# Kernel tuning notes

Measured on AMD Instinct MI355X. Metric: run time of the kernel, lower is better.

The kernel has to match this reference:

```python
import jax, jax.numpy as jnp
import numpy as np

B, S, D, H, L, DFF, LAT, V, N = 256, 64, 512, 8, 6, 2048, 256, 16, 64


def _pe(s, d):
    pos = np.arange(s)[:, None].astype(np.float32)
    div = np.exp(np.arange(0, d, 2).astype(np.float32) * (-np.log(10000.0) / d))
    pe = np.zeros((s, d), np.float32)
    pe[:, 0::2] = np.sin(pos * div)
    pe[:, 1::2] = np.cos(pos * div)
    return jnp.asarray(pe)


def setup_inputs() -> dict:
    key = jax.random.key(0)
    ks = iter(jax.random.split(key, 64))
    def nrm(shape, scale):
        return jax.random.normal(next(ks), shape, jnp.float32) * scale
    d = {}
    d['latent'] = nrm((B, LAT), 1.0)
    ct = jax.random.randint(next(ks), (B, S), 0, V).astype(jnp.float32)
    na = jax.random.randint(next(ks), (B, S), 0, N).astype(jnp.float32)
    nb = jax.random.randint(next(ks), (B, S), 0, N).astype(jnp.float32)
    val = jax.random.normal(next(ks), (B, S), jnp.float32)
    d['teacher_seq'] = jnp.stack([ct, na, nb, val], -1)
    for g in ('gumbel_a', 'gumbel_b'):
        u = jax.random.uniform(next(ks), (B, S, N), jnp.float32, 1e-6, 1.0 - 1e-6)
        d[g] = -jnp.log(-jnp.log(u))
    dq = D // 4
    d['type_emb'] = nrm((V, dq), 0.02)
    d['node_a_emb'] = nrm((N, dq), 0.02)
    d['node_b_emb'] = nrm((N, dq), 0.02)
    d['value_w'] = nrm((dq, 1), 1.0); d['value_b'] = jnp.zeros((dq,))
    d['proj_w'] = nrm((D, D), D ** -0.5); d['proj_b'] = jnp.zeros((D,))
    d['latent_w'] = nrm((D, LAT), LAT ** -0.5); d['latent_b'] = jnp.zeros((D,))
    d['sa_in_w'] = nrm((L, 3 * D, D), D ** -0.5); d['sa_in_b'] = jnp.zeros((L, 3 * D))
    d['sa_out_w'] = nrm((L, D, D), D ** -0.5); d['sa_out_b'] = jnp.zeros((L, D))
    d['ca_q_w'] = nrm((L, D, D), D ** -0.5); d['ca_q_b'] = jnp.zeros((L, D))
    d['ca_kv_w'] = nrm((L, 2 * D, D), D ** -0.5); d['ca_kv_b'] = jnp.zeros((L, 2 * D))
    d['ca_out_w'] = nrm((L, D, D), D ** -0.5); d['ca_out_b'] = jnp.zeros((L, D))
    d['ff1_w'] = nrm((L, DFF, D), D ** -0.5); d['ff1_b'] = jnp.zeros((L, DFF))
    d['ff2_w'] = nrm((L, D, DFF), DFF ** -0.5); d['ff2_b'] = jnp.zeros((L, D))
    for nm in ('ln1', 'ln2', 'ln3'):
        d[nm + '_g'] = jnp.ones((L, D)); d[nm + '_b'] = jnp.zeros((L, D))
    d['type_w'] = nrm((V, D), D ** -0.5); d['type_b'] = jnp.zeros((V,))
    d['na_w'] = nrm((N, D), D ** -0.5); d['na_b'] = jnp.zeros((N,))
    d['val_w'] = nrm((1, D), D ** -0.5); d['val_b'] = jnp.zeros((1,))
    d['nb_w'] = nrm((N, D + N), (D + N) ** -0.5); d['nb_b'] = jnp.zeros((N,))
    return d


def _ln(x, g, b, eps=1e-5):
    m = x.mean(-1, keepdims=True)
    v = jnp.mean((x - m) ** 2, -1, keepdims=True)
    return (x - m) / jnp.sqrt(v + eps) * g + b


def _attn(xq, xkv, wq, bq, wk, bk, wv, bv, wo, bo, mask):
    b, sq, dm = xq.shape
    hd = dm // H
    q = (xq @ wq.T + bq).reshape(b, sq, H, hd)
    k = (xkv @ wk.T + bk).reshape(b, -1, H, hd)
    v = (xkv @ wv.T + bv).reshape(b, -1, H, hd)
    s = jnp.einsum('bqhd,bkhd->bhqk', q, k) / np.sqrt(hd).astype(np.float32)
    if mask is not None:
        s = s + mask
    a = jax.nn.softmax(s, -1)
    o = jnp.einsum('bhqk,bkhd->bqhd', a, v).reshape(b, sq, dm)
    return o @ wo.T + bo


def _forward(latent, teacher_seq, gumbel_a, gumbel_b, type_emb, node_a_emb, node_b_emb,
             value_w, value_b, proj_w, proj_b, latent_w, latent_b,
             sa_in_w, sa_in_b, sa_out_w, sa_out_b,
             ca_q_w, ca_q_b, ca_kv_w, ca_kv_b, ca_out_w, ca_out_b,
             ff1_w, ff1_b, ff2_w, ff2_b,
             ln1_g, ln1_b, ln2_g, ln2_b, ln3_g, ln3_b,
             type_w, type_b, na_w, na_b, val_w, val_b, nb_w, nb_b):
    s = teacher_seq.shape[1]
    memory = (latent @ latent_w.T + latent_b)[:, None, :]  # [B,1,D]
    ct = jnp.clip(teacher_seq[..., 0].astype(jnp.int32), 0, V - 1)
    na = jnp.clip(teacher_seq[..., 1].astype(jnp.int32), 0, N - 1)
    nb = jnp.clip(teacher_seq[..., 2].astype(jnp.int32), 0, N - 1)
    emb = jnp.concatenate([type_emb[ct], node_a_emb[na], node_b_emb[nb],
                           teacher_seq[..., 3:4] @ value_w.T + value_b], -1)
    x = emb @ proj_w.T + proj_b + _pe(s, D)
    mask = jnp.where(jnp.triu(jnp.ones((s, s), bool), 1), -jnp.inf, 0.0)
    for l in range(L):
        wq, wk, wv = jnp.split(sa_in_w[l], 3, 0)
        bq, bk, bv = jnp.split(sa_in_b[l], 3, 0)
        x = _ln(x + _attn(x, x, wq, bq, wk, bk, wv, bv, sa_out_w[l], sa_out_b[l], mask), ln1_g[l], ln1_b[l])
        wkc, wvc = jnp.split(ca_kv_w[l], 2, 0)
        bkc, bvc = jnp.split(ca_kv_b[l], 2, 0)
        x = _ln(x + _attn(x, memory, ca_q_w[l], ca_q_b[l], wkc, bkc, wvc, bvc, ca_out_w[l], ca_out_b[l], None), ln2_g[l], ln2_b[l])
        ff = jax.nn.relu(x @ ff1_w[l].T + ff1_b[l]) @ ff2_w[l].T + ff2_b[l]
        x = _ln(x + ff, ln3_g[l], ln3_b[l])
    type_logits = x @ type_w.T + type_b
    node_a_logits = x @ na_w.T + na_b
    values = x @ val_w.T + val_b
    # gumbel_softmax(logits, tau).argmax == argmax(logits + gumbel) (tau > 0)
    node_a_sample = jnp.argmax(node_a_logits + gumbel_a, -1)
    oh = jax.nn.one_hot(node_a_sample, N, dtype=x.dtype)
    node_b_logits = jnp.concatenate([x, oh], -1) @ nb_w.T + nb_b
    masked = jnp.where(oh > 0, -jnp.inf, node_b_logits)  # node_b != node_a constraint
    node_b_sample = jnp.argmax(masked + gumbel_b, -1)
    sequence = jnp.stack([jnp.argmax(type_logits, -1).astype(x.dtype),
                          node_a_sample.astype(x.dtype),
                          node_b_sample.astype(x.dtype),
                          values[..., 0]], -1)
    return type_logits, node_a_logits, node_b_logits, values, sequence


def reference(latent, teacher_seq, gumbel_a, gumbel_b, type_emb, node_a_emb, node_b_emb,
              value_w, value_b, proj_w, proj_b, latent_w, latent_b,
              sa_in_w, sa_in_b, sa_out_w, sa_out_b,
              ca_q_w, ca_q_b, ca_kv_w, ca_kv_b, ca_out_w, ca_out_b,
              ff1_w, ff1_b, ff2_w, ff2_b,
              ln1_g, ln1_b, ln2_g, ln2_b, ln3_g, ln3_b,
              type_w, type_b, na_w, na_b, val_w, val_b, nb_w, nb_b):
    return _forward(latent, teacher_seq, gumbel_a, gumbel_b, type_emb, node_a_emb, node_b_emb,
                    value_w, value_b, proj_w, proj_b, latent_w, latent_b,
                    sa_in_w, sa_in_b, sa_out_w, sa_out_b,
                    ca_q_w, ca_q_b, ca_kv_w, ca_kv_b, ca_out_w, ca_out_b,
                    ff1_w, ff1_b, ff2_w, ff2_b,
                    ln1_g, ln1_b, ln2_g, ln2_b, ln3_g, ln3_b,
                    type_w, type_b, na_w, na_b, val_w, val_b, nb_w, nb_b)
```

## Files before the change

kernel.cpp:

```cpp
#include <hip/hip_runtime.h>
#include <math.h>

#define BB    256
#define SS    64
#define DD    512
#define HH    8
#define LL    6
#define DFFc  2048
#define LATc  256
#define VVc   16
#define NNODE 64
#define TOK   (BB*SS)

typedef __attribute__((ext_vector_type(8))) _Float16 h8v;
typedef __attribute__((ext_vector_type(4))) float f4v;
typedef __attribute__((ext_vector_type(8))) unsigned short u16x8;

__device__ __forceinline__ float pe_val(int s, int c){
  const float kc = -9.2103403719761836f / 512.0f;
  float div = expf((float)(c & ~1) * kc);
  float arg = (float)s * div;
  return (c & 1) ? cosf(arg) : sinf(arg);
}

__device__ __forceinline__ unsigned short hbits(_Float16 h){
  union { _Float16 h; unsigned short u; } x; x.h = h; return x.u;
}
__device__ __forceinline__ void split4h(float4 v, ushort4& h0, ushort4& h1){
  _Float16 a0 = (_Float16)v.x; float r0 = v.x - (float)a0; h0.x = hbits(a0); h1.x = hbits((_Float16)r0);
  _Float16 a1 = (_Float16)v.y; float r1 = v.y - (float)a1; h0.y = hbits(a1); h1.y = hbits((_Float16)r1);
  _Float16 a2 = (_Float16)v.z; float r2 = v.z - (float)a2; h0.z = hbits(a2); h1.z = hbits((_Float16)r2);
  _Float16 a3 = (_Float16)v.w; float r3 = v.w - (float)a3; h0.w = hbits(a3); h1.w = hbits((_Float16)r3);
}
__device__ __forceinline__ u16x8 pack8(ushort4 a, ushort4 b){
  u16x8 r;
  r[0]=a.x; r[1]=a.y; r[2]=a.z; r[3]=a.w;
  r[4]=b.x; r[5]=b.y; r[6]=b.z; r[7]=b.w;
  return r;
}

__global__ __launch_bounds__(128) void emb_kernel(
    const float* __restrict__ ts, const float* __restrict__ te,
    const float* __restrict__ nae, const float* __restrict__ nbe,
    const float* __restrict__ vw, const float* __restrict__ vb,
    float* __restrict__ emb)
{
  const int tok = blockIdx.x;
  const int d   = threadIdx.x;
  float c0  = ts[(size_t)tok*4 + 0];
  float c1  = ts[(size_t)tok*4 + 1];
  float c2  = ts[(size_t)tok*4 + 2];
  float val = ts[(size_t)tok*4 + 3];
  int ct = min(max((int)c0, 0), VVc - 1);
  int na = min(max((int)c1, 0), NNODE - 1);
  int nb = min(max((int)c2, 0), NNODE - 1);
  float* er = emb + (size_t)tok * DD;
  er[d]       = te [ct*128 + d];
  er[128 + d] = nae[na*128 + d];
  er[256 + d] = nbe[nb*128 + d];
  er[384 + d] = val * vw[d] + vb[d];
}

template<int RELU, int ADDPE>
__global__ __launch_bounds__(256) void gemm_mfma(
    const float* __restrict__ A, const float* __restrict__ W,
    const float* __restrict__ bias, float* __restrict__ Cc,
    int M, int N, int K)
{
  __shared__ __attribute__((aligned(16))) unsigned short Ab[2][128][32];
  __shared__ __attribute__((aligned(16))) unsigned short Bb[2][128][32];
  const int n0 = blockIdx.x * 128;
  const int m0 = blockIdx.y * 128;
  const int t  = threadIdx.x;
  const int lane = t & 63;
  const int wave = t >> 6;
  const int wr = (wave >> 1) * 64;
  const int wc = (wave & 1) * 64;
  const int quad = lane >> 4;
  const int lc   = lane & 15;

  const int srow = t >> 1;
  const int skh  = (t & 1) * 16;

  const int ssw = ((srow ^ (srow >> 2)) & 3);
  const int p0  = (((t & 1) * 2) ^ ssw) * 8;
  const int p1  = ((((t & 1) * 2) ^ ssw) ^ 1) * 8;
  const int fo  = ((quad ^ ((lc ^ (lc >> 2)) & 3))) * 8;

  const float* ap = A + (size_t)(m0 + srow) * K + skh;
  const float* wp = W + (size_t)(n0 + srow) * K + skh;

  f4v acc[4][4];
  #pragma unroll
  for (int i = 0; i < 4; ++i)
    #pragma unroll
    for (int j = 0; j < 4; ++j) acc[i][j] = (f4v){0.f, 0.f, 0.f, 0.f};

  float4 va[4], vb[4];
  #pragma unroll
  for (int q = 0; q < 4; ++q) {
    va[q] = *(const float4*)(ap + q*4);
    vb[q] = *(const float4*)(wp + q*4);
  }

  for (int k0 = 0; k0 < K; k0 += 32) {
    __syncthreads();
    {
      ushort4 h0[4], h1[4];
      #pragma unroll
      for (int q = 0; q < 4; ++q) split4h(va[q], h0[q], h1[q]);
      *(u16x8*)&Ab[0][srow][p0] = pack8(h0[0], h0[1]);
      *(u16x8*)&Ab[0][srow][p1] = pack8(h0[2], h0[3]);
      *(u16x8*)&Ab[1][srow][p0] = pack8(h1[0], h1[1]);
      *(u16x8*)&Ab[1][srow][p1] = pack8(h1[2], h1[3]);
      #pragma unroll
      for (int q = 0; q < 4; ++q) split4h(vb[q], h0[q], h1[q]);
      *(u16x8*)&Bb[0][srow][p0] = pack8(h0[0], h0[1]);
      *(u16x8*)&Bb[0][srow][p1] = pack8(h0[2], h0[3]);
      *(u16x8*)&Bb[1][srow][p0] = pack8(h1[0], h1[1]);
      *(u16x8*)&Bb[1][srow][p1] = pack8(h1[2], h1[3]);
    }
    __syncthreads();
    if (k0 + 32 < K) {
      #pragma unroll
      for (int q = 0; q < 4; ++q) {
        va[q] = *(const float4*)(ap + k0 + 32 + q*4);
        vb[q] = *(const float4*)(wp + k0 + 32 + q*4);
      }
    }
    h8v af[2][4];
    #pragma unroll
    for (int mt = 0; mt < 4; ++mt)
      #pragma unroll
      for (int s = 0; s < 2; ++s)
        af[s][mt] = *(const h8v*)&Ab[s][wr + mt*16 + lc][fo];
    #pragma unroll
    for (int nt = 0; nt < 4; ++nt) {
      h8v b0 = *(const h8v*)&Bb[0][wc + nt*16 + lc][fo];
      h8v b1 = *(const h8v*)&Bb[1][wc + nt*16 + lc][fo];
      #pragma unroll
      for (int mt = 0; mt < 4; ++mt) {
        f4v c = acc[mt][nt];
        c = __builtin_amdgcn_mfma_f32_16x16x32_f16(af[1][mt], b1, c, 0, 0, 0);
        c = __builtin_amdgcn_mfma_f32_16x16x32_f16(af[1][mt], b0, c, 0, 0, 0);
        c = __builtin_amdgcn_mfma_f32_16x16x32_f16(af[0][mt], b1, c, 0, 0, 0);
        c = __builtin_amdgcn_mfma_f32_16x16x32_f16(af[0][mt], b0, c, 0, 0, 0);
        acc[mt][nt] = c;
      }
    }
  }
  #pragma unroll
  for (int mt = 0; mt < 4; ++mt)
    #pragma unroll
    for (int nt = 0; nt < 4; ++nt) {
      int col = n0 + wc + nt*16 + lc;
      float bvv = bias ? bias[col] : 0.f;
      #pragma unroll
      for (int r = 0; r < 4; ++r) {
        int row = m0 + wr + mt*16 + quad*4 + r;
        float v = acc[mt][nt][r] + bvv;
        if (RELU)  v = fmaxf(v, 0.f);
        if (ADDPE) v += pe_val(row & (SS - 1), col);
        Cc[(size_t)row * N + col] = v;
      }
    }
}

template<int RELU, int ADDPE>
__global__ __launch_bounds__(256) void gemm_mfma64(
    const float* __restrict__ A, const float* __restrict__ W,
    const float* __restrict__ bias, float* __restrict__ Cc,
    int M, int N, int K)
{
  __shared__ __attribute__((aligned(16))) unsigned short Ab[2][64][32];
  __shared__ __attribute__((aligned(16))) unsigned short Bb[2][128][32];
  const int n0 = blockIdx.x * 128;
  const int m0 = blockIdx.y * 64;
  const int t  = threadIdx.x;
  const int lane = t & 63;
  const int wave = t >> 6;
  const int wr = (wave >> 1) * 32;
  const int wc = (wave & 1) * 64;
  const int quad = lane >> 4;
  const int lc   = lane & 15;

  const int srow = t >> 1;
  const int skh  = (t & 1) * 16;
  const int ssw  = ((srow ^ (srow >> 2)) & 3);
  const int p0   = (((t & 1) * 2) ^ ssw) * 8;
  const int p1   = ((((t & 1) * 2) ^ ssw) ^ 1) * 8;
  const int arow = t >> 2;
  const int aq   = t & 3;
  const int pA   = (aq ^ ((arow ^ (arow >> 2)) & 3)) * 8;
  const int fo   = ((quad ^ ((lc ^ (lc >> 2)) & 3))) * 8;

  const float* ap = A + (size_t)(m0 + arow) * K + aq*8;
  const float* wp = W + (size_t)(n0 + srow) * K + skh;

  f4v acc[2][4];
  #pragma unroll
  for (int i = 0; i < 2; ++i)
    #pragma unroll
    for (int j = 0; j < 4; ++j) acc[i][j] = (f4v){0.f, 0.f, 0.f, 0.f};

  float4 va[2], vb[4];
  va[0] = *(const float4*)(ap);
  va[1] = *(const float4*)(ap + 4);
  #pragma unroll
  for (int q = 0; q < 4; ++q) vb[q] = *(const float4*)(wp + q*4);

  for (int k0 = 0; k0 < K; k0 += 32) {
    __syncthreads();
    {
      ushort4 h0[4], h1[4];
      split4h(va[0], h0[0], h1[0]);
      split4h(va[1], h0[1], h1[1]);
      *(u16x8*)&Ab[0][arow][pA] = pack8(h0[0], h0[1]);
      *(u16x8*)&Ab[1][arow][pA] = pack8(h1[0], h1[1]);
      #pragma unroll
      for (int q = 0; q < 4; ++q) split4h(vb[q], h0[q], h1[q]);
      *(u16x8*)&Bb[0][srow][p0] = pack8(h0[0], h0[1]);
      *(u16x8*)&Bb[0][srow][p1] = pack8(h0[2], h0[3]);
      *(u16x8*)&Bb[1][srow][p0] = pack8(h1[0], h1[1]);
      *(u16x8*)&Bb[1][srow][p1] = pack8(h1[2], h1[3]);
    }
    __syncthreads();
    if (k0 + 32 < K) {
      va[0] = *(const float4*)(ap + k0 + 32);
      va[1] = *(const float4*)(ap + k0 + 36);
      #pragma unroll
      for (int q = 0; q < 4; ++q) vb[q] = *(const float4*)(wp + k0 + 32 + q*4);
    }
    h8v af[2][2];
    #pragma unroll
    for (int mt = 0; mt < 2; ++mt)
      #pragma unroll
      for (int s = 0; s < 2; ++s)
        af[s][mt] = *(const h8v*)&Ab[s][wr + mt*16 + lc][fo];
    #pragma unroll
    for (int nt = 0; nt < 4; ++nt) {
      h8v b0 = *(const h8v*)&Bb[0][wc + nt*16 + lc][fo];
      h8v b1 = *(const h8v*)&Bb[1][wc + nt*16 + lc][fo];
      #pragma unroll
      for (int mt = 0; mt < 2; ++mt) {
        f4v c = acc[mt][nt];
        c = __builtin_amdgcn_mfma_f32_16x16x32_f16(af[1][mt], b1, c, 0, 0, 0);
        c = __builtin_amdgcn_mfma_f32_16x16x32_f16(af[1][mt], b0, c, 0, 0, 0);
        c = __builtin_amdgcn_mfma_f32_16x16x32_f16(af[0][mt], b1, c, 0, 0, 0);
        c = __builtin_amdgcn_mfma_f32_16x16x32_f16(af[0][mt], b0, c, 0, 0, 0);
        acc[mt][nt] = c;
      }
    }
  }
  #pragma unroll
  for (int mt = 0; mt < 2; ++mt)
    #pragma unroll
    for (int nt = 0; nt < 4; ++nt) {
      int col = n0 + wc + nt*16 + lc;
      float bvv = bias ? bias[col] : 0.f;
      #pragma unroll
      for (int r = 0; r < 4; ++r) {
        int row = m0 + wr + mt*16 + quad*4 + r;
        float v = acc[mt][nt][r] + bvv;
        if (RELU)  v = fmaxf(v, 0.f);
        if (ADDPE) v += pe_val(row & (SS - 1), col);
        Cc[(size_t)row * N + col] = v;
      }
    }
}

__global__ __launch_bounds__(256) void gemm64(
    const float* __restrict__ A, const float* __restrict__ W,
    const float* __restrict__ bias, float* __restrict__ Cc,
    int M, int N, int K)
{
  __shared__ float As[16][64];
  __shared__ float Bs[16][64];
  const int n0 = blockIdx.x * 64;
  const int m0 = blockIdx.y * 64;
  const int t  = threadIdx.x;
  const int tx = t & 15;
  const int ty = t >> 4;
  const int sr = t >> 2;
  const int sk = (t & 3) * 4;

  const float* ap = A + (size_t)(m0 + sr) * K + sk;
  const float* wp = W + (size_t)(n0 + sr) * K + sk;

  float acc[4][4];
  #pragma unroll
  for (int i = 0; i < 4; ++i)
    #pragma unroll
    for (int j = 0; j < 4; ++j) acc[i][j] = 0.f;

  float4 a = *(const float4*)ap;
  float4 b = *(const float4*)wp;
  for (int k0 = 0; k0 < K; k0 += 16) {
    __syncthreads();
    As[sk+0][sr]=a.x; As[sk+1][sr]=a.y; As[sk+2][sr]=a.z; As[sk+3][sr]=a.w;
    Bs[sk+0][sr]=b.x; Bs[sk+1][sr]=b.y; Bs[sk+2][sr]=b.z; Bs[sk+3][sr]=b.w;
    __syncthreads();
    if (k0 + 16 < K) {
      a = *(const float4*)(ap + k0 + 16);
      b = *(const float4*)(wp + k0 + 16);
    }
    #pragma unroll
    for (int kk = 0; kk < 16; ++kk) {
      float4 x = *(const float4*)&As[kk][ty*4];
      float4 y = *(const float4*)&Bs[kk][tx*4];
      float xv[4] = {x.x,x.y,x.z,x.w};
      float yv[4] = {y.x,y.y,y.z,y.w};
      #pragma unroll
      for (int i = 0; i < 4; ++i)
        #pragma unroll
        for (int j = 0; j < 4; ++j)
          acc[i][j] += xv[i] * yv[j];
    }
  }
  #pragma unroll
  for (int i = 0; i < 4; ++i) {
    int r = m0 + ty*4 + i;
    float* cp = Cc + (size_t)r * N + n0 + tx*4;
    float4 o;
    o.x = acc[i][0] + (bias ? bias[n0+tx*4+0] : 0.f);
    o.y = acc[i][1] + (bias ? bias[n0+tx*4+1] : 0.f);
    o.z = acc[i][2] + (bias ? bias[n0+tx*4+2] : 0.f);
    o.w = acc[i][3] + (bias ? bias[n0+tx*4+3] : 0.f);
    *(float4*)cp = o;
  }
}

__global__ __launch_bounds__(64) void attn_kernel(
    const float* __restrict__ qkv, float* __restrict__ out)
{
  const int b = blockIdx.x >> 3;
  const int h = blockIdx.x & 7;
  const int lane = threadIdx.x;
  __shared__ float4 ks[64][16];
  __shared__ float4 vs[64][16];
  const float* base = qkv + (size_t)(b*SS + lane) * (3*DD);
  #pragma unroll
  for (int dd = 0; dd < 16; ++dd) {
    ks[lane][dd] = *(const float4*)(base + DD     + h*64 + dd*4);
    vs[lane][dd] = *(const float4*)(base + 2*DD   + h*64 + dd*4);
  }
  float4 q4[16];
  #pragma unroll
  for (int dd = 0; dd < 16; ++dd) q4[dd] = *(const float4*)(base + h*64 + dd*4);
  __syncthreads();

  float s[64];
  float m = -1e30f;
  #pragma unroll
  for (int tk = 0; tk < 64; ++tk) {
    float acc = 0.f;
    #pragma unroll
    for (int dd = 0; dd < 16; ++dd) {
      float4 kv = ks[tk][dd];
      acc += q4[dd].x*kv.x + q4[dd].y*kv.y + q4[dd].z*kv.z + q4[dd].w*kv.w;
    }
    acc *= 0.125f;
    s[tk] = acc;
    if (tk <= lane && acc > m) m = acc;
  }
  float4 o4[16];
  #pragma unroll
  for (int dd = 0; dd < 16; ++dd) { o4[dd].x = 0.f; o4[dd].y = 0.f; o4[dd].z = 0.f; o4[dd].w = 0.f; }
  float l = 0.f;
  #pragma unroll
  for (int tk = 0; tk < 64; ++tk) {
    float w = (tk <= lane) ? expf(s[tk] - m) : 0.f;
    l += w;
    #pragma unroll
    for (int dd = 0; dd < 16; ++dd) {
      float4 vv = vs[tk][dd];
      o4[dd].x += w*vv.x; o4[dd].y += w*vv.y; o4[dd].z += w*vv.z; o4[dd].w += w*vv.w;
    }
  }
  float inv = 1.f / l;
  float* op = out + (size_t)(b*SS + lane) * DD + h*64;
  #pragma unroll
  for (int dd = 0; dd < 16; ++dd) {
    float4 vv; vv.x = o4[dd].x*inv; vv.y = o4[dd].y*inv; vv.z = o4[dd].z*inv; vv.w = o4[dd].w*inv;
    *(float4*)(op + dd*4) = vv;
  }
}

__global__ __launch_bounds__(256) void ln_kernel(
    float* __restrict__ x, const float* __restrict__ y,
    const float* __restrict__ g, const float* __restrict__ b, int ybcast)
{
  const int tok  = blockIdx.x * 4 + (threadIdx.x >> 6);
  const int lane = threadIdx.x & 63;
  float* xr = x + (size_t)tok * DD;
  const float* yr = y + (size_t)(ybcast ? (tok >> 6) : tok) * DD;
  const int c0 = lane * 8;
  float4 v0 = *(const float4*)(xr + c0);
  float4 v1 = *(const float4*)(xr + c0 + 4);
  float4 y0 = *(const float4*)(yr + c0);
  float4 y1 = *(const float4*)(yr + c0 + 4);
  float v[8] = {v0.x+y0.x, v0.y+y0.y, v0.z+y0.z, v0.w+y0.w,
                v1.x+y1.x, v1.y+y1.y, v1.z+y1.z, v1.w+y1.w};
  float sum = 0.f;
  #pragma unroll
  for (int i = 0; i < 8; ++i) sum += v[i];
  #pragma unroll
  for (int off = 32; off; off >>= 1) sum += __shfl_xor(sum, off);
  float mean = sum * (1.f / 512.f);
  float ss = 0.f;
  #pragma unroll
  for (int i = 0; i < 8; ++i) { float d = v[i] - mean; ss += d*d; }
  #pragma unroll
  for (int off = 32; off; off >>= 1) ss += __shfl_xor(ss, off);
  float rinv = 1.f / sqrtf(ss * (1.f / 512.f) + 1e-5f);
  float4 g0 = *(const float4*)(g + c0);
  float4 g1 = *(const float4*)(g + c0 + 4);
  float4 b0 = *(const float4*)(b + c0);
  float4 b1 = *(const float4*)(b + c0 + 4);
  float4 o0, o1;
  o0.x = (v[0]-mean)*rinv*g0.x + b0.x;
  o0.y = (v[1]-mean)*rinv*g0.y + b0.y;
  o0.z = (v[2]-mean)*rinv*g0.z + b0.z;
  o0.w = (v[3]-mean)*rinv*g0.w + b0.w;
  o1.x = (v[4]-mean)*rinv*g1.x + b1.x;
  o1.y = (v[5]-mean)*rinv*g1.y + b1.y;
  o1.z = (v[6]-mean)*rinv*g1.z + b1.z;
  o1.w = (v[7]-mean)*rinv*g1.w + b1.w;
  *(float4*)(xr + c0)     = o0;
  *(float4*)(xr + c0 + 4) = o1;
}

__global__ __launch_bounds__(128) void build_whead(
    const float* __restrict__ tw, const float* __restrict__ tb,
    const float* __restrict__ nw, const float* __restrict__ nab,
    const float* __restrict__ bw, const float* __restrict__ bbb,
    const float* __restrict__ vw, const float* __restrict__ vb,
    float* __restrict__ Wh, float* __restrict__ Bh)
{
  const int row = blockIdx.x;
  const int t   = threadIdx.x;
  const float* src = nullptr; float bias = 0.f;
  if      (row < 16)  { src = tw + (size_t)row*512;        bias = tb[row]; }
  else if (row < 80)  { src = nw + (size_t)(row-16)*512;   bias = nab[row-16]; }
  else if (row < 144) { src = bw + (size_t)(row-80)*576;   bias = bbb[row-80]; }
  else if (row == 144){ src = vw;                          bias = vb[0]; }
  float* dst = Wh + (size_t)row*512;
  const int c = t * 4;
  float4 v;
  if (src) v = *(const float4*)(src + c);
  else { v.x = 0.f; v.y = 0.f; v.z = 0.f; v.w = 0.f; }
  *(float4*)(dst + c) = v;
  if (t == 0) Bh[row] = bias;
}

__device__ __forceinline__ void argmax64(float& v, int& idx){
  #pragma unroll
  for (int off = 1; off < 64; off <<= 1) {
    float ov = __shfl_xor(v, off);
    int   oi = __shfl_xor(idx, off);
    if (ov > v || (ov == v && oi < idx)) { v = ov; idx = oi; }
  }
}

__global__ __launch_bounds__(64) void head_finalize(
    const float* __restrict__ LG, const float* __restrict__ nb_w,
    const float* __restrict__ gum_a, const float* __restrict__ gum_b,
    float* __restrict__ out)
{
  const int O_NA  = TOK*VVc;
  const int O_NB  = O_NA + TOK*NNODE;
  const int O_VAL = O_NB + TOK*NNODE;
  const int O_SEQ = O_VAL + TOK;
  const int tok  = blockIdx.x;
  const int lane = threadIdx.x;
  const float* lg = LG + (size_t)tok * 256;

  float tl = (lane < VVc) ? lg[lane] : -INFINITY;
  if (lane < VVc) out[(size_t)tok*VVc + lane] = tl;
  float tv = tl; int ti = lane;
  argmax64(tv, ti);

  float nl = lg[16 + lane];
  out[O_NA + (size_t)tok*NNODE + lane] = nl;
  float av = nl + gum_a[(size_t)tok*NNODE + lane];
  int ai = lane;
  argmax64(av, ai);

  float bl = lg[80 + lane] + nb_w[(size_t)lane*576 + 512 + ai];
  out[O_NB + (size_t)tok*NNODE + lane] = bl;
  float mb = (lane == ai) ? -INFINITY : bl;
  mb += gum_b[(size_t)tok*NNODE + lane];
  int bi = lane;
  argmax64(mb, bi);

  if (lane == 0) {
    float value = lg[144];
    out[O_VAL + tok]               = value;
    out[O_SEQ + (size_t)tok*4 + 0] = (float)ti;
    out[O_SEQ + (size_t)tok*4 + 1] = (float)ai;
    out[O_SEQ + (size_t)tok*4 + 2] = (float)bi;
    out[O_SEQ + (size_t)tok*4 + 3] = value;
  }
}

__device__ __forceinline__ float dot512(const float* __restrict__ xs, const float* __restrict__ w){
  float s = 0.f;
  #pragma unroll 8
  for (int k = 0; k < 512; k += 4) {
    float4 u = *(const float4*)(w + k);
    s += xs[k]*u.x + xs[k+1]*u.y + xs[k+2]*u.z + xs[k+3]*u.w;
  }
  return s;
}

__global__ __launch_bounds__(64) void head_kernel(
    const float* __restrict__ x,
    const float* __restrict__ type_w, const float* __restrict__ type_b,
    const float* __restrict__ na_w,  const float* __restrict__ na_b,
    const float* __restrict__ vw,    const float* __restrict__ vb,
    const float* __restrict__ nb_w,  const float* __restrict__ nb_b,
    const float* __restrict__ gum_a, const float* __restrict__ gum_b,
    float* __restrict__ out)
{
  const int O_NA  = TOK*VVc;
  const int O_NB  = O_NA + TOK*NNODE;
  const int O_VAL = O_NB + TOK*NNODE;
  const int O_SEQ = O_VAL + TOK;
  const int tok  = blockIdx.x;
  const int lane = threadIdx.x;
  __shared__ float xs[512];
  const float* xr = x + (size_t)tok * DD;
  *(float4*)&xs[lane*8]     = *(const float4*)(xr + lane*8);
  *(float4*)&xs[lane*8 + 4] = *(const float4*)(xr + lane*8 + 4);
  __syncthreads();

  float pv = 0.f;
  #pragma unroll
  for (int i = 0; i < 8; ++i) pv += xs[lane*8 + i] * vw[lane*8 + i];
  #pragma unroll
  for (int off = 32; off; off >>= 1) pv += __shfl_xor(pv, off);
  float value = pv + vb[0];

  float tl = -INFINITY;
  if (lane < VVc) {
    tl = type_b[lane] + dot512(xs, type_w + (size_t)lane*512);
    out[(size_t)tok*VVc + lane] = tl;
  }
  float tv = tl; int ti = lane;
  argmax64(tv, ti);

  float nl = na_b[lane] + dot512(xs, na_w + (size_t)lane*512);
  out[O_NA + (size_t)tok*NNODE + lane] = nl;
  float av = nl + gum_a[(size_t)tok*NNODE + lane];
  int ai = lane;
  argmax64(av, ai);

  const float* wr = nb_w + (size_t)lane * 576;
  float bl = nb_b[lane] + dot512(xs, wr) + wr[512 + ai];
  out[O_NB + (size_t)tok*NNODE + lane] = bl;
  float mb = (lane == ai) ? -INFINITY : bl;
  mb += gum_b[(size_t)tok*NNODE + lane];
  int bi = lane;
  argmax64(mb, bi);

  if (lane == 0) {
    out[O_VAL + tok]               = value;
    out[O_SEQ + (size_t)tok*4 + 0] = (float)ti;
    out[O_SEQ + (size_t)tok*4 + 1] = (float)ai;
    out[O_SEQ + (size_t)tok*4 + 2] = (float)bi;
    out[O_SEQ + (size_t)tok*4 + 3] = value;
  }
}

extern "C" void kernel_launch(void* const* d_in, const int* in_sizes, int n_in,
                              void* d_out, int out_size, void* d_ws, size_t ws_size,
                              hipStream_t stream)
{
  (void)in_sizes; (void)n_in; (void)out_size;
  const float* latent   = (const float*)d_in[0];
  const float* teacher  = (const float*)d_in[1];
  const float* gum_a    = (const float*)d_in[2];
  const float* gum_b    = (const float*)d_in[3];
  const float* type_emb = (const float*)d_in[4];
  const float* nae      = (const float*)d_in[5];
  const float* nbe      = (const float*)d_in[6];
  const float* value_w  = (const float*)d_in[7];
  const float* value_b  = (const float*)d_in[8];
  const float* proj_w   = (const float*)d_in[9];
  const float* proj_b   = (const float*)d_in[10];
  const float* latent_w = (const float*)d_in[11];
  const float* latent_b = (const float*)d_in[12];
  const float* sa_in_w  = (const float*)d_in[13];
  const float* sa_in_b  = (const float*)d_in[14];
  const float* sa_out_w = (const float*)d_in[15];
  const float* sa_out_b = (const float*)d_in[16];
  const float* ca_kv_w  = (const float*)d_in[19];
  const float* ca_kv_b  = (const float*)d_in[20];
  const float* ca_out_w = (const float*)d_in[21];
  const float* ca_out_b = (const float*)d_in[22];
  const float* ff1_w    = (const float*)d_in[23];
  const float* ff1_b    = (const float*)d_in[24];
  const float* ff2_w    = (const float*)d_in[25];
  const float* ff2_b    = (const float*)d_in[26];
  const float* ln1_g    = (const float*)d_in[27];
  const float* ln1_b    = (const float*)d_in[28];
  const float* ln2_g    = (const float*)d_in[29];
  const float* ln2_b    = (const float*)d_in[30];
  const float* ln3_g    = (const float*)d_in[31];
  const float* ln3_b    = (const float*)d_in[32];
  const float* type_w   = (const float*)d_in[33];
  const float* type_b   = (const float*)d_in[34];
  const float* na_w     = (const float*)d_in[35];
  const float* na_b     = (const float*)d_in[36];
  const float* val_w    = (const float*)d_in[37];
  const float* val_b    = (const float*)d_in[38];
  const float* nb_w     = (const float*)d_in[39];
  const float* nb_b     = (const float*)d_in[40];

  int C = 128;
  for (int c = 16384; c >= 128; c >>= 1) {
    size_t need = ((size_t)8781824 + (size_t)3072 * c) * 4;
    if (need <= ws_size) { C = c; break; }
  }
  const int NCH = TOK / C;

  float* ws   = (float*)d_ws;
  float* X    = ws;
  float* U    = X    + (size_t)TOK*DD;
  float* P1   = U    + (size_t)2048*C;
  float* P2   = P1   + (size_t)C*DD;
  float* MEM  = P2   + (size_t)C*DD;
  float* CAV  = MEM  + (size_t)BB*DD;
  float* CAO  = CAV  + (size_t)BB*DD;
  float* out = (float*)d_out;

  for (int c = 0; c < NCH; ++c) {
    emb_kernel<<<C, 128, 0, stream>>>(teacher + (size_t)c*C*4, type_emb, nae, nbe, value_w, value_b, U);
    gemm_mfma64<0,1><<<dim3(DD/128, C/64), 256, 0, stream>>>(U, proj_w, proj_b, X + (size_t)c*C*DD, C, DD, DD);
  }
  gemm64<<<dim3(DD/64, BB/64), 256, 0, stream>>>(latent, latent_w, latent_b, MEM, BB, DD, LATc);

  for (int l = 0; l < LL; ++l) {
    const float* w_qkv = sa_in_w  + (size_t)l*3*DD*DD;
    const float* b_qkv = sa_in_b  + (size_t)l*3*DD;
    const float* w_so  = sa_out_w + (size_t)l*DD*DD;
    const float* b_so  = sa_out_b + (size_t)l*DD;
    const float* w_cv  = ca_kv_w  + (size_t)l*2*DD*DD + (size_t)DD*DD;
    const float* b_cv  = ca_kv_b  + (size_t)l*2*DD + DD;
    const float* w_co  = ca_out_w + (size_t)l*DD*DD;
    const float* b_co  = ca_out_b + (size_t)l*DD;
    const float* w_f1  = ff1_w    + (size_t)l*DFFc*DD;
    const float* b_f1  = ff1_b    + (size_t)l*DFFc;
    const float* w_f2  = ff2_w    + (size_t)l*DD*DFFc;
    const float* b_f2  = ff2_b    + (size_t)l*DD;

    for (int c = 0; c < NCH; ++c) {
      float* Xc = X + (size_t)c*C*DD;
      gemm_mfma<0,0><<<dim3(3*DD/128, C/128), 256, 0, stream>>>(Xc, w_qkv, b_qkv, U, C, 3*DD, DD);
      attn_kernel<<<(C/SS)*HH, 64, 0, stream>>>(U, P1);
      gemm_mfma64<0,0><<<dim3(DD/128, C/64), 256, 0, stream>>>(P1, w_so, b_so, P2, C, DD, DD);
      ln_kernel<<<C/4, 256, 0, stream>>>(Xc, P2, ln1_g + (size_t)l*DD, ln1_b + (size_t)l*DD, 0);
    }
    gemm64<<<dim3(DD/64, BB/64), 256, 0, stream>>>(MEM, w_cv, b_cv, CAV, BB, DD, DD);
    gemm64<<<dim3(DD/64, BB/64), 256, 0, stream>>>(CAV, w_co, b_co, CAO, BB, DD, DD);
    ln_kernel<<<TOK/4, 256, 0, stream>>>(X, CAO, ln2_g + (size_t)l*DD, ln2_b + (size_t)l*DD, 1);
    for (int c = 0; c < NCH; ++c) {
      float* Xc = X + (size_t)c*C*DD;
      gemm_mfma<1,0><<<dim3(DFFc/128, C/128), 256, 0, stream>>>(Xc, w_f1, b_f1, U, C, DFFc, DD);
      gemm_mfma64<0,0><<<dim3(DD/128, C/64), 256, 0, stream>>>(U, w_f2, b_f2, P1, C, DD, DFFc);
      ln_kernel<<<C/4, 256, 0, stream>>>(Xc, P1, ln3_g + (size_t)l*DD, ln3_b + (size_t)l*DD, 0);
    }
  }

  if (C >= 2048) {
    float* Wh = CAV;
    float* Bh = CAO;
    float* LG = U;
    build_whead<<<256, 128, 0, stream>>>(type_w, type_b, na_w, na_b, nb_w, nb_b, val_w, val_b, Wh, Bh);
    gemm_mfma64<0,0><<<dim3(256/128, TOK/64), 256, 0, stream>>>(X, Wh, Bh, LG, TOK, 256, 512);
    head_finalize<<<TOK, 64, 0, stream>>>(LG, nb_w, gum_a, gum_b, out);
  } else {
    head_kernel<<<TOK, 64, 0, stream>>>(X, type_w, type_b, na_w, na_b, val_w, val_b,
                                        nb_w, nb_b, gum_a, gum_b, out);
  }
}
```

Baseline: 3.956 ms.

## Add intra-block split-K GEMM with 128x128 tiles for N=512 projections

Adds a 512-thread GEMM kernel where two 256-thread halves each process half of K on a 128x128 output tile, then reduce the partial sums through LDS before the epilogue. It replaces the 64x128-tile kernel for the input projection, self-attention output projection and FF2. The goal is more A/B reuse per tile while keeping enough waves in flight for the narrow N=512 outputs. In exchange it uses a larger LDS footprint, adds a reduction step, and doubles register pressure per block.

```diff
diff --git a/kernel.cpp b/kernel.cpp
--- a/kernel.cpp
+++ b/kernel.cpp
@@ -164,6 +164,137 @@
         Cc[(size_t)row * N + col] = v;
       }
     }
+}
+
+template<int RELU, int ADDPE>
+__global__ __launch_bounds__(512) void gemm_sk(
+    const float* __restrict__ A, const float* __restrict__ W,
+    const float* __restrict__ bias, float* __restrict__ Cc,
+    int M, int N, int K)
+{
+  __shared__ __attribute__((aligned(16))) unsigned short LDSu[2][2][2][128][32];
+  const int Kh = K >> 1;
+  const int n0 = blockIdx.x * 128;
+  const int m0 = blockIdx.y * 128;
+  const int t  = threadIdx.x;
+  const int kz = t >> 8;
+  const int ht = t & 255;
+  const int lane = t & 63;
+  const int w4   = (t >> 6) & 3;
+  const int wr = (w4 >> 1) * 64;
+  const int wc = (w4 & 1) * 64;
+  const int quad = lane >> 4;
+  const int lc   = lane & 15;
+
+  const int srow = ht >> 1;
+  const int skh  = (ht & 1) * 16;
+  const int ssw  = ((srow ^ (srow >> 2)) & 3);
+  const int p0   = (((ht & 1) * 2) ^ ssw) * 8;
+  const int p1   = ((((ht & 1) * 2) ^ ssw) ^ 1) * 8;
+  const int fo   = ((quad ^ ((lc ^ (lc >> 2)) & 3))) * 8;
+
+  const float* ap = A + (size_t)(m0 + srow) * K + kz * Kh + skh;
+  const float* wp = W + (size_t)(n0 + srow) * K + kz * Kh + skh;
+
+  f4v acc[4][4];
+  #pragma unroll
+  for (int i = 0; i < 4; ++i)
+    #pragma unroll
+    for (int j = 0; j < 4; ++j) acc[i][j] = (f4v){0.f, 0.f, 0.f, 0.f};
+
+  float4 va[4], vb[4];
+  #pragma unroll
+  for (int q = 0; q < 4; ++q) {
+    va[q] = *(const float4*)(ap + q*4);
+    vb[q] = *(const float4*)(wp + q*4);
+  }
+
+  for (int k0 = 0; k0 < Kh; k0 += 32) {
+    __syncthreads();
+    {
+      ushort4 h0[4], h1[4];
+      #pragma unroll
+      for (int q = 0; q < 4; ++q) split4h(va[q], h0[q], h1[q]);
+      *(u16x8*)&LDSu[0][kz][0][srow][p0] = pack8(h0[0], h0[1]);
+      *(u16x8*)&LDSu[0][kz][0][srow][p1] = pack8(h0[2], h0[3]);
+      *(u16x8*)&LDSu[0][kz][1][srow][p0] = pack8(h1[0], h1[1]);
+      *(u16x8*)&LDSu[0][kz][1][srow][p1] = pack8(h1[2], h1[3]);
+      #pragma unroll
+      for (int q = 0; q < 4; ++q) split4h(vb[q], h0[q], h1[q]);
+      *(u16x8*)&LDSu[1][kz][0][srow][p0] = pack8(h0[0], h0[1]);
+      *(u16x8*)&LDSu[1][kz][0][srow][p1] = pack8(h0[2], h0[3]);
+      *(u16x8*)&LDSu[1][kz][1][srow][p0] = pack8(h1[0], h1[1]);
+      *(u16x8*)&LDSu[1][kz][1][srow][p1] = pack8(h1[2], h1[3]);
+    }
+    __syncthreads();
+    if (k0 + 32 < Kh) {
+      #pragma unroll
+      for (int q = 0; q < 4; ++q) {
+        va[q] = *(const float4*)(ap + k0 + 32 + q*4);
+        vb[q] = *(const float4*)(wp + k0 + 32 + q*4);
+      }
+    }
+    h8v af[2][4];
+    #pragma unroll
+    for (int mt = 0; mt < 4; ++mt)
+      #pragma unroll
+      for (int s = 0; s < 2; ++s)
+        af[s][mt] = *(const h8v*)&LDSu[0][kz][s][wr + mt*16 + lc][fo];
+    #pragma unroll
+    for (int nt = 0; nt < 4; ++nt) {
+      h8v b0 = *(const h8v*)&LDSu[1][kz][0][wc + nt*16 + lc][fo];
+      h8v b1 = *(const h8v*)&LDSu[1][kz][1][wc + nt*16 + lc][fo];
+      #pragma unroll
+      for (int mt = 0; mt < 4; ++mt) {
+        f4v c = acc[mt][nt];
+        c = __builtin_amdgcn_mfma_f32_16x16x32_f16(af[1][mt], b1, c, 0, 0, 0);
+        c = __builtin_amdgcn_mfma_f32_16x16x32_f16(af[1][mt], b0, c, 0, 0, 0);
+        c = __builtin_amdgcn_mfma_f32_16x16x32_f16(af[0][mt], b1, c, 0, 0, 0);
+        c = __builtin_amdgcn_mfma_f32_16x16x32_f16(af[0][mt], b0, c, 0, 0, 0);
+        acc[mt][nt] = c;
+      }
+    }
+  }
+
+  __syncthreads();
+  float* cb = (float*)LDSu;
+  if (kz == 1) {
+    float* my = cb + (size_t)w4 * 4096 + lane * 64;
+    #pragma unroll
+    for (int mt = 0; mt < 4; ++mt)
+      #pragma unroll
+      for (int nt = 0; nt < 4; ++nt) {
+        int gs = (mt*4 + nt) ^ (lane & 7);
+        *(f4v*)&my[gs * 4] = acc[mt][nt];
+      }
+  }
+  __syncthreads();
+  if (kz == 0) {
+    const float* my = cb + (size_t)w4 * 4096 + lane * 64;
+    #pragma unroll
+    for (int mt = 0; mt < 4; ++mt)
+      #pragma unroll
+      for (int nt = 0; nt < 4; ++nt) {
+        int gs = (mt*4 + nt) ^ (lane & 7);
+        f4v o = *(const f4v*)&my[gs * 4];
+        acc[mt][nt] += o;
+      }
+    #pragma unroll
+    for (int mt = 0; mt < 4; ++mt)
+      #pragma unroll
+      for (int nt = 0; nt < 4; ++nt) {
+        int col = n0 + wc + nt*16 + lc;
+        float bvv = bias ? bias[col] : 0.f;
+        #pragma unroll
+        for (int r = 0; r < 4; ++r) {
+          int row = m0 + wr + mt*16 + quad*4 + r;
+          float v = acc[mt][nt][r] + bvv;
+          if (RELU)  v = fmaxf(v, 0.f);
+          if (ADDPE) v += pe_val(row & (SS - 1), col);
+          Cc[(size_t)row * N + col] = v;
+        }
+      }
+  }
 }
 
 template<int RELU, int ADDPE>
@@ -636,7 +767,7 @@
 
   for (int c = 0; c < NCH; ++c) {
     emb_kernel<<<C, 128, 0, stream>>>(teacher + (size_t)c*C*4, type_emb, nae, nbe, value_w, value_b, U);
-    gemm_mfma64<0,1><<<dim3(DD/128, C/64), 256, 0, stream>>>(U, proj_w, proj_b, X + (size_t)c*C*DD, C, DD, DD);
+    gemm_sk<0,1><<<dim3(DD/128, C/128), 512, 0, stream>>>(U, proj_w, proj_b, X + (size_t)c*C*DD, C, DD, DD);
   }
   gemm64<<<dim3(DD/64, BB/64), 256, 0, stream>>>(latent, latent_w, latent_b, MEM, BB, DD, LATc);
 
@@ -658,7 +789,7 @@
       float* Xc = X + (size_t)c*C*DD;
       gemm_mfma<0,0><<<dim3(3*DD/128, C/128), 256, 0, stream>>>(Xc, w_qkv, b_qkv, U, C, 3*DD, DD);
       attn_kernel<<<(C/SS)*HH, 64, 0, stream>>>(U, P1);
-      gemm_mfma64<0,0><<<dim3(DD/128, C/64), 256, 0, stream>>>(P1, w_so, b_so, P2, C, DD, DD);
+      gemm_sk<0,0><<<dim3(DD/128, C/128), 512, 0, stream>>>(P1, w_so, b_so, P2, C, DD, DD);
       ln_kernel<<<C/4, 256, 0, stream>>>(Xc, P2, ln1_g + (size_t)l*DD, ln1_b + (size_t)l*DD, 0);
     }
     gemm64<<<dim3(DD/64, BB/64), 256, 0, stream>>>(MEM, w_cv, b_cv, CAV, BB, DD, DD);
@@ -667,7 +798,7 @@
     for (int c = 0; c < NCH; ++c) {
       float* Xc = X + (size_t)c*C*DD;
       gemm_mfma<1,0><<<dim3(DFFc/128, C/128), 256, 0, stream>>>(Xc, w_f1, b_f1, U, C, DFFc, DD);
-      gemm_mfma64<0,0><<<dim3(DD/128, C/64), 256, 0, stream>>>(U, w_f2, b_f2, P1, C, DD, DFFc);
+      gemm_sk<0,0><<<dim3(DD/128, C/128), 512, 0, stream>>>(U, w_f2, b_f2, P1, C, DD, DFFc);
       ln_kernel<<<C/4, 256, 0, stream>>>(Xc, P1, ln3_g + (size_t)l*DD, ln3_b + (size_t)l*DD, 0);
     }
   }
```

After: 4.105 ms. 3.8% more time.
